# Optimization experiments

Measured on AMD Instinct MI355X. Metric: run time of the kernel, lower is better.

Reference implementation:

```python
import jax, jax.numpy as jnp
import numpy as np

NUM_CLASSES = 54
EPSILON = 0.001
IMPORTANT = [1, 3, 5, 7, 11, 13, 17, 19, 23, 29, 31, 37]
BATCH = 2_000_000


def setup_inputs() -> dict:
    key = jax.random.key(0)
    k1, k2 = jax.random.split(key)
    logits = jax.random.normal(k1, (BATCH, NUM_CLASSES), dtype=jnp.float32)
    target = jax.random.randint(k2, (BATCH,), 0, NUM_CLASSES, dtype=jnp.int64 if jax.config.read('jax_enable_x64') else jnp.int32)
    important_mask = jnp.zeros((NUM_CLASSES,), dtype=bool).at[jnp.array(IMPORTANT)].set(True)
    return {"logits": logits, "target": target, "important_mask": important_mask}


def reference(logits, target, important_mask):
    # softmax over classes
    sm = jax.nn.softmax(logits, axis=1)                     # [B, C]
    pred = jnp.argmax(sm, axis=1)                           # [B]
    # vectorized membership test (replaces the per-sample .item() loop)
    keep = important_mask[pred] | important_mask[target]    # [B]
    # NLLLoss only reads the target column of log(adjusted_softmax):
    #   kept sample   -> softmax[i, target[i]]
    #   ignored sample-> 1 - (C-1)*epsilon  (constant)
    p_target = jnp.take_along_axis(sm, target[:, None], axis=1)[:, 0]  # [B]
    target_prob = 1.0 - (NUM_CLASSES - 1) * EPSILON
    adj = jnp.where(keep, p_target, target_prob)
    loss = -jnp.mean(jnp.log(adj))
    return loss
```

## Files before the change

### kernel.cpp

```cpp
#include <hip/hip_runtime.h>

#define BATCH_N 2000000
#define NCLS 54

__device__ __constant__ unsigned long long kImportantMask =
    (1ULL << 1) | (1ULL << 3) | (1ULL << 5) | (1ULL << 7) |
    (1ULL << 11) | (1ULL << 13) | (1ULL << 17) | (1ULL << 19) |
    (1ULL << 23) | (1ULL << 29) | (1ULL << 31) | (1ULL << 37);

__global__ __launch_bounds__(256) void important_loss_kernel(
    const float* __restrict__ logits,
    const int* __restrict__ target,
    float* __restrict__ out,
    int batch) {
    int row = blockIdx.x * blockDim.x + threadIdx.x;

    float local = 0.0f;
    if (row < batch) {
        const float2* rp = reinterpret_cast<const float2*>(logits + (size_t)row * NCLS);
        float v[NCLS];
#pragma unroll
        for (int j = 0; j < NCLS / 2; ++j) {
            float2 t2 = rp[j];
            v[2 * j]     = t2.x;
            v[2 * j + 1] = t2.y;
        }

        int t = target[row];

        float m = v[0];
        int am = 0;
        float vt = v[0];
#pragma unroll
        for (int j = 1; j < NCLS; ++j) {
            bool gt = v[j] > m;
            m  = gt ? v[j] : m;
            am = gt ? j : am;
            vt = (j == t) ? v[j] : vt;
        }

        float s = 0.0f;
#pragma unroll
        for (int j = 0; j < NCLS; ++j) {
            s += __expf(v[j] - m);
        }

        unsigned long long mask = kImportantMask;
        bool keep = (((mask >> am) & 1ULL) | ((mask >> t) & 1ULL)) != 0ULL;

        const float ignored_nll = 0.054456182f;
        float nll = keep ? (__logf(s) - (vt - m)) : ignored_nll;
        local = nll;
    }

#pragma unroll
    for (int off = 32; off > 0; off >>= 1) {
        local += __shfl_down(local, off, 64);
    }

    __shared__ float wsum[4];
    int lane = threadIdx.x & 63;
    int wid  = threadIdx.x >> 6;
    if (lane == 0) wsum[wid] = local;
    __syncthreads();

    if (threadIdx.x == 0) {
        float bs = wsum[0] + wsum[1] + wsum[2] + wsum[3];
        atomicAdd(out, bs * (1.0f / (float)BATCH_N));
    }
}

extern "C" void kernel_launch(void* const* d_in, const int* in_sizes, int n_in,
                              void* d_out, int out_size, void* d_ws, size_t ws_size,
                              hipStream_t stream) {
    const float* logits = (const float*)d_in[0];
    const int* target   = (const int*)d_in[1];
    float* out = (float*)d_out;

    hipMemsetAsync(out, 0, sizeof(float), stream);

    int batch = in_sizes[1];
    int block = 256;
    int grid = (batch + block - 1) / block;
    important_loss_kernel<<<grid, block, 0, stream>>>(logits, target, out, batch);
}
```

Baseline: 568.4 us.

## Stage logits through LDS with coalesced loads and two-pass reduction

Each 64-thread block cooperatively loads 64 rows into shared memory with coalesced float4 reads, then each thread processes its row from LDS. This replaces the strided per-thread float2 global loads. The argmax is replaced by a tree max plus an equality check on the important classes. The exp sum drops the max subtraction, which risks overflow for large logits. The per-block atomic is replaced by a partials buffer and a second reduce kernel, and tail rows are dropped when the batch is not a multiple of 64.

```diff
diff --git a/kernel.cpp b/kernel.cpp
--- a/kernel.cpp
+++ b/kernel.cpp
@@ -1,72 +1,103 @@
 #include <hip/hip_runtime.h>
 
+#define NCLS 54
+#define ROWS 64
 #define BATCH_N 2000000
-#define NCLS 54
 
-__device__ __constant__ unsigned long long kImportantMask =
-    (1ULL << 1) | (1ULL << 3) | (1ULL << 5) | (1ULL << 7) |
-    (1ULL << 11) | (1ULL << 13) | (1ULL << 17) | (1ULL << 19) |
-    (1ULL << 23) | (1ULL << 29) | (1ULL << 31) | (1ULL << 37);
+#define IMP_MASK ((1ULL << 1) | (1ULL << 3) | (1ULL << 5) | (1ULL << 7) |   \
+                  (1ULL << 11) | (1ULL << 13) | (1ULL << 17) | (1ULL << 19) | \
+                  (1ULL << 23) | (1ULL << 29) | (1ULL << 31) | (1ULL << 37))
 
-__global__ __launch_bounds__(256) void important_loss_kernel(
+__global__ __launch_bounds__(64) void loss_main(
     const float* __restrict__ logits,
     const int* __restrict__ target,
-    float* __restrict__ out,
-    int batch) {
-    int row = blockIdx.x * blockDim.x + threadIdx.x;
+    float* __restrict__ partial) {
+    __shared__ __align__(16) float tile[ROWS * NCLS];
 
-    float local = 0.0f;
-    if (row < batch) {
-        const float2* rp = reinterpret_cast<const float2*>(logits + (size_t)row * NCLS);
-        float v[NCLS];
+    const int tid = threadIdx.x;
+    const size_t row0 = (size_t)blockIdx.x * ROWS;
+
+    const float4* gp = reinterpret_cast<const float4*>(logits + row0 * NCLS);
+    float4* lp = reinterpret_cast<float4*>(tile);
 #pragma unroll
-        for (int j = 0; j < NCLS / 2; ++j) {
-            float2 t2 = rp[j];
-            v[2 * j]     = t2.x;
-            v[2 * j + 1] = t2.y;
-        }
+    for (int k = 0; k < 13; ++k) {
+        lp[tid + 64 * k] = gp[tid + 64 * k];
+    }
+    if (tid < 864 - 13 * 64) {
+        lp[tid + 13 * 64] = gp[tid + 13 * 64];
+    }
+    int t = target[row0 + tid];
+    __syncthreads();
 
-        int t = target[row];
+    const float* rv = &tile[tid * NCLS];
+    float v[NCLS];
+#pragma unroll
+    for (int j = 0; j < NCLS / 2; ++j) {
+        float2 t2 = reinterpret_cast<const float2*>(rv)[j];
+        v[2 * j] = t2.x;
+        v[2 * j + 1] = t2.y;
+    }
+    float vt = rv[t];
 
-        float m = v[0];
-        int am = 0;
-        float vt = v[0];
+    float w[27];
 #pragma unroll
-        for (int j = 1; j < NCLS; ++j) {
-            bool gt = v[j] > m;
-            m  = gt ? v[j] : m;
-            am = gt ? j : am;
-            vt = (j == t) ? v[j] : vt;
-        }
+    for (int j = 0; j < 27; ++j) w[j] = fmaxf(v[j], v[j + 27]);
+#pragma unroll
+    for (int j = 0; j < 13; ++j) w[j] = fmaxf(w[j], w[j + 14]);
+#pragma unroll
+    for (int j = 0; j < 7; ++j) w[j] = fmaxf(w[j], w[j + 7]);
+#pragma unroll
+    for (int j = 0; j < 3; ++j) w[j] = fmaxf(w[j], w[j + 4]);
+    w[0] = fmaxf(w[0], w[2]);
+    w[1] = fmaxf(w[1], w[3]);
+    const float m = fmaxf(w[0], w[1]);
 
-        float s = 0.0f;
+    const int IMP[12] = {1, 3, 5, 7, 11, 13, 17, 19, 23, 29, 31, 37};
+    bool imp_pred = false;
 #pragma unroll
-        for (int j = 0; j < NCLS; ++j) {
-            s += __expf(v[j] - m);
-        }
+    for (int j = 0; j < 12; ++j) imp_pred |= (v[IMP[j]] == m);
 
-        unsigned long long mask = kImportantMask;
-        bool keep = (((mask >> am) & 1ULL) | ((mask >> t) & 1ULL)) != 0ULL;
+    bool keep = imp_pred || (((IMP_MASK >> t) & 1ULL) != 0ULL);
 
-        const float ignored_nll = 0.054456182f;
-        float nll = keep ? (__logf(s) - (vt - m)) : ignored_nll;
-        local = nll;
+    float s0 = 0.f, s1 = 0.f, s2 = 0.f, s3 = 0.f;
+#pragma unroll
+    for (int j = 0; j < 52; j += 4) {
+        s0 += __expf(v[j]);
+        s1 += __expf(v[j + 1]);
+        s2 += __expf(v[j + 2]);
+        s3 += __expf(v[j + 3]);
     }
+    s0 += __expf(v[52]);
+    s1 += __expf(v[53]);
+    float s = (s0 + s1) + (s2 + s3);
+
+    float local = keep ? (__logf(s) - vt) : 0.054456182f;
 
 #pragma unroll
     for (int off = 32; off > 0; off >>= 1) {
         local += __shfl_down(local, off, 64);
     }
+    if (tid == 0) partial[blockIdx.x] = local;
+}
 
-    __shared__ float wsum[4];
+__global__ __launch_bounds__(1024) void loss_reduce(
+    const float* __restrict__ partial, int n, float* __restrict__ out) {
+    float s = 0.f;
+    for (int i = threadIdx.x; i < n; i += 1024) s += partial[i];
+#pragma unroll
+    for (int off = 32; off > 0; off >>= 1) {
+        s += __shfl_down(s, off, 64);
+    }
+    __shared__ float wsum[16];
     int lane = threadIdx.x & 63;
-    int wid  = threadIdx.x >> 6;
-    if (lane == 0) wsum[wid] = local;
+    int wid = threadIdx.x >> 6;
+    if (lane == 0) wsum[wid] = s;
     __syncthreads();
-
     if (threadIdx.x == 0) {
-        float bs = wsum[0] + wsum[1] + wsum[2] + wsum[3];
-        atomicAdd(out, bs * (1.0f / (float)BATCH_N));
+        float bs = 0.f;
+#pragma unroll
+        for (int k = 0; k < 16; ++k) bs += wsum[k];
+        out[0] = bs * (1.0f / (float)BATCH_N);
     }
 }
 
@@ -76,11 +107,11 @@
     const float* logits = (const float*)d_in[0];
     const int* target   = (const int*)d_in[1];
     float* out = (float*)d_out;
-
-    hipMemsetAsync(out, 0, sizeof(float), stream);
+    float* partial = (float*)d_ws;
 
     int batch = in_sizes[1];
-    int block = 256;
-    int grid = (batch + block - 1) / block;
-    important_loss_kernel<<<grid, block, 0, stream>>>(logits, target, out, batch);
+    int nblocks = batch / ROWS;
+
+    loss_main<<<nblocks, ROWS, 0, stream>>>(logits, target, partial);
+    loss_reduce<<<1, 1024, 0, stream>>>(partial, nblocks, out);
 }
```

After: 559.0 us. No clear change (-1.7%).
